# Kernel tuning notes

Hardware: AMD Instinct MI355X
Metric: run time of the kernel (lower is better)

The kernel has to match this reference:

```python
import jax, jax.numpy as jnp
import numpy as np
from jax import lax

DIM = 1024
BATCH = 16
WIDTH = 2048
DECAY = 0.99


def setup_inputs() -> dict:
    key = jax.random.key(0)
    k1, k2, k3, k4 = jax.random.split(key, 4)
    scale = 1.0 / np.sqrt(DIM)
    x = jax.random.normal(k1, (BATCH, WIDTH, DIM), dtype=jnp.float32)
    state = jnp.zeros((BATCH, DIM), dtype=jnp.float32)
    Wv = jax.random.normal(k2, (DIM, DIM), dtype=jnp.float32) * scale
    Wr = jax.random.normal(k3, (DIM, DIM), dtype=jnp.float32) * scale
    Wc = jax.random.normal(k4, (DIM, DIM), dtype=jnp.float32) * scale
    return {"x": x, "state": state, "Wv": Wv, "Wr": Wr, "Wc": Wc}


def reference(x, state, Wv, Wr, Wc):
    # x: [B, W, D], state: [B, D]; fixed-decay RWKV recurrence along width.
    decay = jnp.asarray(DECAY, dtype=x.dtype)
    one_minus = jnp.asarray(1.0, dtype=x.dtype) - decay
    v = jnp.einsum('bwd,de->bwe', x, Wv)                 # value projection
    r = jax.nn.sigmoid(jnp.einsum('bwd,de->bwe', x, Wr))  # receptance

    # scan over width (time) axis: elems shaped [W, B, D]
    def step(s_prev, inp):
        v_t, r_t, x_t = inp
        s_curr = decay * s_prev + one_minus * v_t
        y_t = x_t + r_t * s_curr
        return s_curr, y_t

    elems = (jnp.swapaxes(v, 0, 1), jnp.swapaxes(r, 0, 1), jnp.swapaxes(x, 0, 1))
    new_state, y_t = lax.scan(step, state, elems)
    y = jnp.swapaxes(y_t, 0, 1)                          # [B, W, D]
    y = y + jnp.einsum('bwd,de->bwe', y, Wc)             # minimal channel mix
    return y, new_state
```

## Files before the change

kernel.cpp:

```cpp
#include <hip/hip_runtime.h>
#include <hip/hip_bf16.h>
#include <math.h>


#define MROWS 32768
#define NCHUNK 16
#define CHUNKL 128
#define DECAY_F 0.99f
#define OM_F 0.01f

typedef __attribute__((ext_vector_type(8))) short short8;
typedef __attribute__((ext_vector_type(4))) float floatx4;

using bf16 = __hip_bfloat16;
using bf162 = __hip_bfloat162;

__device__ __forceinline__ void async_copy16(const bf16* g, bf16* l) {
  __builtin_amdgcn_global_load_lds(
      (const __attribute__((address_space(1))) unsigned int*)g,
      (__attribute__((address_space(3))) unsigned int*)l, 16, 0, 0);
}

__global__ void prep_x(const float* __restrict__ X, bf16* __restrict__ Xb) {
  const int idx = blockIdx.x * 256 + threadIdx.x;
  const float4 v = ((const float4*)X)[idx];
  union { ushort4 u; bf16 h[4]; } pk;
  pk.h[0] = __float2bfloat16(v.x);
  pk.h[1] = __float2bfloat16(v.y);
  pk.h[2] = __float2bfloat16(v.z);
  pk.h[3] = __float2bfloat16(v.w);
  ((ushort4*)Xb)[idx] = pk.u;
}

__global__ void prep_weights(const float* __restrict__ Wv,
                             const float* __restrict__ Wr,
                             const float* __restrict__ Wc,
                             bf16* __restrict__ WT) {
  __shared__ float tile[32][33];
  const int bk = blockIdx.x * 32;
  const int bn = blockIdx.y * 32;
  const float* src;
  int nbase = bn;
  if (bn < 1024)      { src = Wv; }
  else if (bn < 2048) { src = Wr; nbase = bn - 1024; }
  else                { src = Wc; nbase = bn - 2048; }
  const int tx = threadIdx.x;
  const int ty = threadIdx.y;
  #pragma unroll
  for (int i = ty; i < 32; i += 8)
    tile[i][tx] = src[(size_t)(bk + i) * 1024 + nbase + tx];
  __syncthreads();
  #pragma unroll
  for (int i = ty; i < 32; i += 8)
    WT[(size_t)(bn + i) * 1024 + bk + tx] = __float2bfloat16(tile[tx][i]);
}

__global__ __launch_bounds__(256, 3) void gemm_vr(const bf16* __restrict__ Xb,
                                                  const bf16* __restrict__ WT,
                                                  bf16* __restrict__ Vout,
                                                  bf16* __restrict__ Rout) {
  __shared__ bf16 As[128][32];
  __shared__ bf16 Bs[128][32];
  const int t = threadIdx.x;
  const int id = blockIdx.x;
  const int grp = id >> 3, xcd = id & 7;
  const int mt = ((grp >> 4) << 3) | xcd;
  const int nt = grp & 15;
  const int m0 = mt * 128;
  const int lane = t & 63, wave = t >> 6;
  const int wm = wave >> 1, wn = wave & 1;
  const int ln15 = lane & 15, qd = lane >> 4;

  const bf16* Asrc = Xb + (size_t)m0 * 1024;
  const bf16* Bsrc = WT + (size_t)(nt * 128) * 1024;

  const int srow = lane >> 2;
  const int skb  = (lane & 3) * 8;

  floatx4 acc[4][4];
  #pragma unroll
  for (int i = 0; i < 4; ++i)
    #pragma unroll
    for (int j = 0; j < 4; ++j) acc[i][j] = (floatx4){0.f, 0.f, 0.f, 0.f};

  for (int k0 = 0; k0 < 1024; k0 += 32) {
    #pragma unroll
    for (int s = 0; s < 2; ++s) {
      const int seg = wave * 2 + s;
      const size_t roff = (size_t)(seg * 16 + srow) * 1024 + k0 + skb;
      async_copy16(&Asrc[roff], &As[seg * 16][0]);
      async_copy16(&Bsrc[roff], &Bs[seg * 16][0]);
    }
    __syncthreads();
    short8 fa[4], fb[4];
    #pragma unroll
    for (int tm = 0; tm < 4; ++tm)
      fa[tm] = *(const short8*)&As[wm * 64 + tm * 16 + ln15][qd * 8];
    #pragma unroll
    for (int tn = 0; tn < 4; ++tn)
      fb[tn] = *(const short8*)&Bs[wn * 64 + tn * 16 + ln15][qd * 8];
    #pragma unroll
    for (int tm = 0; tm < 4; ++tm)
      #pragma unroll
      for (int tn = 0; tn < 4; ++tn)
        acc[tm][tn] = __builtin_amdgcn_mfma_f32_16x16x32_bf16(
            fa[tm], fb[tn], acc[tm][tn], 0, 0, 0);
    __syncthreads();
  }

  const bool isr = (nt >= 8);
  bf16* outp = isr ? Rout : Vout;
  const int nc0 = (nt & 7) * 128;
  #pragma unroll
  for (int tm = 0; tm < 4; ++tm) {
    #pragma unroll
    for (int i = 0; i < 4; ++i) {
      const int m_g = m0 + wm * 64 + tm * 16 + qd * 4 + i;
      const size_t rowoff = (size_t)m_g * 1024 + nc0;
      #pragma unroll
      for (int tn = 0; tn < 4; ++tn) {
        float cv = acc[tm][tn][i];
        if (isr) cv = 1.0f / (1.0f + __expf(-cv));
        outp[rowoff + wn * 64 + tn * 16 + ln15] = __float2bfloat16(cv);
      }
    }
  }
}

__global__ void scan_partial(const bf16* __restrict__ V, float* __restrict__ sl) {
  const int idx = blockIdx.x * 256 + threadIdx.x;
  const int d2 = idx & 511;
  const int c = (idx >> 9) & 15;
  const int b = idx >> 13;
  const bf162* V2 = (const bf162*)V;
  const size_t base = (size_t)(b * 2048 + c * 128) * 512 + d2;
  float s0 = 0.f, s1 = 0.f;
  for (int w = 0; w < CHUNKL; ++w) {
    const bf162 v = V2[base + (size_t)w * 512];
    s0 = DECAY_F * s0 + OM_F * __bfloat162float(v.x);
    s1 = DECAY_F * s1 + OM_F * __bfloat162float(v.y);
  }
  const int o = (b * 16 + c) * 1024 + d2 * 2;
  sl[o] = s0;
  sl[o + 1] = s1;
}

__global__ void scan_chunk(const float* __restrict__ state,
                           const float* __restrict__ sl,
                           float* __restrict__ sin_,
                           float* __restrict__ state_out,
                           float decayL) {
  const int idx = blockIdx.x * 256 + threadIdx.x;
  const int d = idx & 1023;
  const int b = idx >> 10;
  float s = state[idx];
  #pragma unroll
  for (int c = 0; c < NCHUNK; ++c) {
    const int o = (b * 16 + c) * 1024 + d;
    sin_[o] = s;
    s = decayL * s + sl[o];
  }
  state_out[idx] = s;
}

__global__ void scan_apply(const bf16* __restrict__ Xb,
                           const bf16* __restrict__ R,
                           const float* __restrict__ sin_,
                           bf16* __restrict__ VY) {
  const int idx = blockIdx.x * 256 + threadIdx.x;
  const int d2 = idx & 511;
  const int c = (idx >> 9) & 15;
  const int b = idx >> 13;
  const bf162* R2 = (const bf162*)R;
  const bf162* X2 = (const bf162*)Xb;
  bf162* VY2 = (bf162*)VY;
  const size_t base = (size_t)(b * 2048 + c * 128) * 512 + d2;
  const int so = (b * 16 + c) * 1024 + d2 * 2;
  float s0 = sin_[so], s1 = sin_[so + 1];
  for (int w = 0; w < CHUNKL; ++w) {
    const size_t off = base + (size_t)w * 512;
    const bf162 v = VY2[off];
    const bf162 r = R2[off];
    const bf162 xx = X2[off];
    s0 = DECAY_F * s0 + OM_F * __bfloat162float(v.x);
    s1 = DECAY_F * s1 + OM_F * __bfloat162float(v.y);
    const float y0 = __bfloat162float(xx.x) + __bfloat162float(r.x) * s0;
    const float y1 = __bfloat162float(xx.y) + __bfloat162float(r.y) * s1;
    bf162 o;
    o.x = __float2bfloat16(y0);
    o.y = __float2bfloat16(y1);
    VY2[off] = o;
  }
}

__global__ __launch_bounds__(256, 3) void gemm_mix(const bf16* __restrict__ Yt,
                                                   const bf16* __restrict__ WcT,
                                                   float* __restrict__ Out) {
  __shared__ bf16 As[128][32];
  __shared__ bf16 Bs[128][32];
  const int t = threadIdx.x;
  const int id = blockIdx.x;
  const int grp = id >> 3, xcd = id & 7;
  const int mt = ((grp >> 3) << 3) | xcd;
  const int nt = grp & 7;
  const int m0 = mt * 128;
  const int nc0 = nt * 128;
  const int lane = t & 63, wave = t >> 6;
  const int wm = wave >> 1, wn = wave & 1;
  const int ln15 = lane & 15, qd = lane >> 4;

  const bf16* Asrc = Yt + (size_t)m0 * 1024;
  const bf16* Bsrc = WcT + (size_t)nc0 * 1024;

  const int srow = lane >> 2;
  const int skb  = (lane & 3) * 8;

  floatx4 acc[4][4];
  #pragma unroll
  for (int i = 0; i < 4; ++i)
    #pragma unroll
    for (int j = 0; j < 4; ++j) acc[i][j] = (floatx4){0.f, 0.f, 0.f, 0.f};

  for (int k0 = 0; k0 < 1024; k0 += 32) {
    #pragma unroll
    for (int s = 0; s < 2; ++s) {
      const int seg = wave * 2 + s;
      const size_t roff = (size_t)(seg * 16 + srow) * 1024 + k0 + skb;
      async_copy16(&Asrc[roff], &As[seg * 16][0]);
      async_copy16(&Bsrc[roff], &Bs[seg * 16][0]);
    }
    __syncthreads();
    short8 fa[4], fb[4];
    #pragma unroll
    for (int tm = 0; tm < 4; ++tm)
      fa[tm] = *(const short8*)&As[wm * 64 + tm * 16 + ln15][qd * 8];
    #pragma unroll
    for (int tn = 0; tn < 4; ++tn)
      fb[tn] = *(const short8*)&Bs[wn * 64 + tn * 16 + ln15][qd * 8];
    #pragma unroll
    for (int tm = 0; tm < 4; ++tm)
      #pragma unroll
      for (int tn = 0; tn < 4; ++tn)
        acc[tm][tn] = __builtin_amdgcn_mfma_f32_16x16x32_bf16(
            fa[tm], fb[tn], acc[tm][tn], 0, 0, 0);
    __syncthreads();
  }

  #pragma unroll
  for (int tm = 0; tm < 4; ++tm) {
    #pragma unroll
    for (int i = 0; i < 4; ++i) {
      const int m_g = m0 + wm * 64 + tm * 16 + qd * 4 + i;
      const size_t rowoff = (size_t)m_g * 1024 + nc0;
      #pragma unroll
      for (int tn = 0; tn < 4; ++tn) {
        const size_t o = rowoff + wn * 64 + tn * 16 + ln15;
        Out[o] = __bfloat162float(Yt[o]) + acc[tm][tn][i];
      }
    }
  }
}

extern "C" void kernel_launch(void* const* d_in, const int* in_sizes, int n_in,
                              void* d_out, int out_size, void* d_ws, size_t ws_size,
                              hipStream_t stream) {
  const float* x     = (const float*)d_in[0];
  const float* state = (const float*)d_in[1];
  const float* Wv    = (const float*)d_in[2];
  const float* Wr    = (const float*)d_in[3];
  const float* Wc    = (const float*)d_in[4];

  float* y_out = (float*)d_out;
  float* state_out = y_out + (size_t)MROWS * 1024;

  char* ws = (char*)d_ws;
  bf16* WT   = (bf16*)ws;
  bf16* Xb   = (bf16*)(ws + ((size_t)6 << 20));
  bf16* Vbuf = (bf16*)(ws + ((size_t)70 << 20));
  bf16* Rbuf = (bf16*)(ws + ((size_t)134 << 20));
  float* sl  = (float*)(ws + ((size_t)198 << 20));
  float* sin_ = (float*)(ws + ((size_t)199 << 20));
  bf16* WcT = WT + (size_t)2048 * 1024;

  const float decayL = (float)pow(0.99, (double)CHUNKL);

  prep_x<<<32768, 256, 0, stream>>>(x, Xb);
  prep_weights<<<dim3(32, 96), dim3(32, 8), 0, stream>>>(Wv, Wr, Wc, WT);
  gemm_vr<<<4096, 256, 0, stream>>>(Xb, WT, Vbuf, Rbuf);
  scan_partial<<<512, 256, 0, stream>>>(Vbuf, sl);
  scan_chunk<<<64, 256, 0, stream>>>(state, sl, sin_, state_out, decayL);
  scan_apply<<<512, 256, 0, stream>>>(Xb, Rbuf, sin_, Vbuf);
  gemm_mix<<<2048, 256, 0, stream>>>(Vbuf, WcT, y_out);
}
```

Baseline: 529.4 us.

## Quantize value/receptance GEMM inputs to FP8 with scaled MFMA and widen scan vectors

Converts x and Wv/Wr to FP8 (weights pre-scaled by 16, undone via the MFMA scale operand) and switches gemm_vr to the 16x16x128 f8f6f4 scaled MFMA with a K-step of 128 and an XOR-swizzled LDS layout. This halves GEMM input bytes and raises matrix throughput per instruction. The scan kernels now process four channels per thread and scan_apply reads the fp32 x directly instead of the bf16 copy. The trade-off is a larger numeric error from FP8 inputs, which may approach the tolerance.

```diff
diff --git a/kernel.cpp b/kernel.cpp
--- a/kernel.cpp
+++ b/kernel.cpp
@@ -11,31 +11,40 @@
 
 typedef __attribute__((ext_vector_type(8))) short short8;
 typedef __attribute__((ext_vector_type(4))) float floatx4;
+typedef __attribute__((ext_vector_type(8))) int i32x8;
 
 using bf16 = __hip_bfloat16;
-using bf162 = __hip_bfloat162;
-
-__device__ __forceinline__ void async_copy16(const bf16* g, bf16* l) {
+
+__device__ __forceinline__ void async_copy16(const void* g, void* l) {
   __builtin_amdgcn_global_load_lds(
       (const __attribute__((address_space(1))) unsigned int*)g,
       (__attribute__((address_space(3))) unsigned int*)l, 16, 0, 0);
 }
 
-__global__ void prep_x(const float* __restrict__ X, bf16* __restrict__ Xb) {
+__device__ __forceinline__ float b2f(unsigned short u) {
+  union { unsigned int i; float f; } t; t.i = ((unsigned int)u) << 16; return t.f;
+}
+__device__ __forceinline__ unsigned short f2bu(float f) {
+  bf16 h = __float2bfloat16(f);
+  return *reinterpret_cast<unsigned short*>(&h);
+}
+
+__global__ void prep_x8(const float* __restrict__ X, unsigned char* __restrict__ Xq) {
   const int idx = blockIdx.x * 256 + threadIdx.x;
-  const float4 v = ((const float4*)X)[idx];
-  union { ushort4 u; bf16 h[4]; } pk;
-  pk.h[0] = __float2bfloat16(v.x);
-  pk.h[1] = __float2bfloat16(v.y);
-  pk.h[2] = __float2bfloat16(v.z);
-  pk.h[3] = __float2bfloat16(v.w);
-  ((ushort4*)Xb)[idx] = pk.u;
+  const float4 v0 = ((const float4*)X)[idx * 2];
+  const float4 v1 = ((const float4*)X)[idx * 2 + 1];
+  int p0 = __builtin_amdgcn_cvt_pk_fp8_f32(v0.x, v0.y, 0, false);
+  p0 = __builtin_amdgcn_cvt_pk_fp8_f32(v0.z, v0.w, p0, true);
+  int p1 = __builtin_amdgcn_cvt_pk_fp8_f32(v1.x, v1.y, 0, false);
+  p1 = __builtin_amdgcn_cvt_pk_fp8_f32(v1.z, v1.w, p1, true);
+  ((uint2*)Xq)[idx] = make_uint2((unsigned)p0, (unsigned)p1);
 }
 
 __global__ void prep_weights(const float* __restrict__ Wv,
                              const float* __restrict__ Wr,
                              const float* __restrict__ Wc,
-                             bf16* __restrict__ WT) {
+                             unsigned char* __restrict__ Wq8,
+                             bf16* __restrict__ WcT) {
   __shared__ float tile[32][33];
   const int bk = blockIdx.x * 32;
   const int bn = blockIdx.y * 32;
@@ -50,17 +59,25 @@
   for (int i = ty; i < 32; i += 8)
     tile[i][tx] = src[(size_t)(bk + i) * 1024 + nbase + tx];
   __syncthreads();
-  #pragma unroll
-  for (int i = ty; i < 32; i += 8)
-    WT[(size_t)(bn + i) * 1024 + bk + tx] = __float2bfloat16(tile[tx][i]);
-}
-
-__global__ __launch_bounds__(256, 3) void gemm_vr(const bf16* __restrict__ Xb,
-                                                  const bf16* __restrict__ WT,
+  if (bn < 2048) {
+    #pragma unroll
+    for (int i = ty; i < 32; i += 8) {
+      const int p = __builtin_amdgcn_cvt_pk_fp8_f32(tile[tx][i] * 16.0f, 0.f, 0, false);
+      Wq8[(size_t)(bn + i) * 1024 + bk + tx] = (unsigned char)(p & 0xff);
+    }
+  } else {
+    #pragma unroll
+    for (int i = ty; i < 32; i += 8)
+      WcT[(size_t)(bn - 2048 + i) * 1024 + bk + tx] = __float2bfloat16(tile[tx][i]);
+  }
+}
+
+__global__ __launch_bounds__(256, 3) void gemm_vr(const unsigned char* __restrict__ Xq,
+                                                  const unsigned char* __restrict__ Wq8,
                                                   bf16* __restrict__ Vout,
                                                   bf16* __restrict__ Rout) {
-  __shared__ bf16 As[128][32];
-  __shared__ bf16 Bs[128][32];
+  __shared__ uint4 As4[1024];
+  __shared__ uint4 Bs4[1024];
   const int t = threadIdx.x;
   const int id = blockIdx.x;
   const int grp = id >> 3, xcd = id & 7;
@@ -68,14 +85,15 @@
   const int nt = grp & 15;
   const int m0 = mt * 128;
   const int lane = t & 63, wave = t >> 6;
-  const int wm = wave >> 1, wn = wave & 1;
+  const int wm = (wave >> 1) * 64, wn = (wave & 1) * 64;
   const int ln15 = lane & 15, qd = lane >> 4;
-
-  const bf16* Asrc = Xb + (size_t)m0 * 1024;
-  const bf16* Bsrc = WT + (size_t)(nt * 128) * 1024;
-
-  const int srow = lane >> 2;
-  const int skb  = (lane & 3) * 8;
+  const int swz = ln15 & 7;
+
+  const unsigned char* Asrc = Xq + (size_t)m0 * 1024;
+  const unsigned char* Bsrc = Wq8 + (size_t)(nt * 128) * 1024;
+
+  const int r8 = lane >> 3;
+  const int xcol = ((lane & 7) ^ r8) * 16;
 
   floatx4 acc[4][4];
   #pragma unroll
@@ -83,28 +101,38 @@
     #pragma unroll
     for (int j = 0; j < 4; ++j) acc[i][j] = (floatx4){0.f, 0.f, 0.f, 0.f};
 
-  for (int k0 = 0; k0 < 1024; k0 += 32) {
-    #pragma unroll
-    for (int s = 0; s < 2; ++s) {
-      const int seg = wave * 2 + s;
-      const size_t roff = (size_t)(seg * 16 + srow) * 1024 + k0 + skb;
-      async_copy16(&Asrc[roff], &As[seg * 16][0]);
-      async_copy16(&Bsrc[roff], &Bs[seg * 16][0]);
+  for (int k0 = 0; k0 < 1024; k0 += 128) {
+    #pragma unroll
+    for (int c = 0; c < 4; ++c) {
+      const int rbase = wave * 32 + c * 8;
+      const size_t goff = (size_t)(rbase + r8) * 1024 + k0 + xcol;
+      async_copy16(Asrc + goff, (char*)&As4[rbase * 8]);
+      async_copy16(Bsrc + goff, (char*)&Bs4[rbase * 8]);
     }
     __syncthreads();
-    short8 fa[4], fb[4];
-    #pragma unroll
-    for (int tm = 0; tm < 4; ++tm)
-      fa[tm] = *(const short8*)&As[wm * 64 + tm * 16 + ln15][qd * 8];
-    #pragma unroll
-    for (int tn = 0; tn < 4; ++tn)
-      fb[tn] = *(const short8*)&Bs[wn * 64 + tn * 16 + ln15][qd * 8];
+    i32x8 fa[4], fb[4];
+    #pragma unroll
+    for (int tm = 0; tm < 4; ++tm) {
+      const int row = wm + tm * 16 + ln15;
+      const uint4 lo = As4[row * 8 + ((qd * 2) ^ swz)];
+      const uint4 hi = As4[row * 8 + ((qd * 2 + 1) ^ swz)];
+      fa[tm][0] = lo.x; fa[tm][1] = lo.y; fa[tm][2] = lo.z; fa[tm][3] = lo.w;
+      fa[tm][4] = hi.x; fa[tm][5] = hi.y; fa[tm][6] = hi.z; fa[tm][7] = hi.w;
+    }
+    #pragma unroll
+    for (int tn = 0; tn < 4; ++tn) {
+      const int row = wn + tn * 16 + ln15;
+      const uint4 lo = Bs4[row * 8 + ((qd * 2) ^ swz)];
+      const uint4 hi = Bs4[row * 8 + ((qd * 2 + 1) ^ swz)];
+      fb[tn][0] = lo.x; fb[tn][1] = lo.y; fb[tn][2] = lo.z; fb[tn][3] = lo.w;
+      fb[tn][4] = hi.x; fb[tn][5] = hi.y; fb[tn][6] = hi.z; fb[tn][7] = hi.w;
+    }
     #pragma unroll
     for (int tm = 0; tm < 4; ++tm)
       #pragma unroll
       for (int tn = 0; tn < 4; ++tn)
-        acc[tm][tn] = __builtin_amdgcn_mfma_f32_16x16x32_bf16(
-            fa[tm], fb[tn], acc[tm][tn], 0, 0, 0);
+        acc[tm][tn] = __builtin_amdgcn_mfma_scale_f32_16x16x128_f8f6f4(
+            fa[tm], fb[tn], acc[tm][tn], 0, 0, 0, 127, 0, 123);
     __syncthreads();
   }
 
@@ -115,13 +143,13 @@
   for (int tm = 0; tm < 4; ++tm) {
     #pragma unroll
     for (int i = 0; i < 4; ++i) {
-      const int m_g = m0 + wm * 64 + tm * 16 + qd * 4 + i;
+      const int m_g = m0 + wm + tm * 16 + qd * 4 + i;
       const size_t rowoff = (size_t)m_g * 1024 + nc0;
       #pragma unroll
       for (int tn = 0; tn < 4; ++tn) {
         float cv = acc[tm][tn][i];
         if (isr) cv = 1.0f / (1.0f + __expf(-cv));
-        outp[rowoff + wn * 64 + tn * 16 + ln15] = __float2bfloat16(cv);
+        outp[rowoff + wn + tn * 16 + ln15] = __float2bfloat16(cv);
       }
     }
   }
@@ -129,20 +157,20 @@
 
 __global__ void scan_partial(const bf16* __restrict__ V, float* __restrict__ sl) {
   const int idx = blockIdx.x * 256 + threadIdx.x;
-  const int d2 = idx & 511;
-  const int c = (idx >> 9) & 15;
-  const int b = idx >> 13;
-  const bf162* V2 = (const bf162*)V;
-  const size_t base = (size_t)(b * 2048 + c * 128) * 512 + d2;
-  float s0 = 0.f, s1 = 0.f;
+  const int d4 = idx & 255;
+  const int c = (idx >> 8) & 15;
+  const int b = idx >> 12;
+  const ushort4* V4 = (const ushort4*)V;
+  const size_t base = (size_t)(b * 2048 + c * 128) * 256 + d4;
+  float s0 = 0.f, s1 = 0.f, s2 = 0.f, s3 = 0.f;
   for (int w = 0; w < CHUNKL; ++w) {
-    const bf162 v = V2[base + (size_t)w * 512];
-    s0 = DECAY_F * s0 + OM_F * __bfloat162float(v.x);
-    s1 = DECAY_F * s1 + OM_F * __bfloat162float(v.y);
-  }
-  const int o = (b * 16 + c) * 1024 + d2 * 2;
-  sl[o] = s0;
-  sl[o + 1] = s1;
+    const ushort4 v = V4[base + (size_t)w * 256];
+    s0 = DECAY_F * s0 + OM_F * b2f(v.x);
+    s1 = DECAY_F * s1 + OM_F * b2f(v.y);
+    s2 = DECAY_F * s2 + OM_F * b2f(v.z);
+    s3 = DECAY_F * s3 + OM_F * b2f(v.w);
+  }
+  ((float4*)sl)[(b * 16 + c) * 256 + d4] = make_float4(s0, s1, s2, s3);
 }
 
 __global__ void scan_chunk(const float* __restrict__ state,
@@ -163,33 +191,34 @@
   state_out[idx] = s;
 }
 
-__global__ void scan_apply(const bf16* __restrict__ Xb,
+__global__ void scan_apply(const float* __restrict__ X,
                            const bf16* __restrict__ R,
                            const float* __restrict__ sin_,
                            bf16* __restrict__ VY) {
   const int idx = blockIdx.x * 256 + threadIdx.x;
-  const int d2 = idx & 511;
-  const int c = (idx >> 9) & 15;
-  const int b = idx >> 13;
-  const bf162* R2 = (const bf162*)R;
-  const bf162* X2 = (const bf162*)Xb;
-  bf162* VY2 = (bf162*)VY;
-  const size_t base = (size_t)(b * 2048 + c * 128) * 512 + d2;
-  const int so = (b * 16 + c) * 1024 + d2 * 2;
-  float s0 = sin_[so], s1 = sin_[so + 1];
+  const int d4 = idx & 255;
+  const int c = (idx >> 8) & 15;
+  const int b = idx >> 12;
+  const ushort4* R4 = (const ushort4*)R;
+  const float4* X4 = (const float4*)X;
+  ushort4* VY4 = (ushort4*)VY;
+  const size_t base = (size_t)(b * 2048 + c * 128) * 256 + d4;
+  float4 s = ((const float4*)sin_)[(b * 16 + c) * 256 + d4];
   for (int w = 0; w < CHUNKL; ++w) {
-    const size_t off = base + (size_t)w * 512;
-    const bf162 v = VY2[off];
-    const bf162 r = R2[off];
-    const bf162 xx = X2[off];
-    s0 = DECAY_F * s0 + OM_F * __bfloat162float(v.x);
-    s1 = DECAY_F * s1 + OM_F * __bfloat162float(v.y);
-    const float y0 = __bfloat162float(xx.x) + __bfloat162float(r.x) * s0;
-    const float y1 = __bfloat162float(xx.y) + __bfloat162float(r.y) * s1;
-    bf162 o;
-    o.x = __float2bfloat16(y0);
-    o.y = __float2bfloat16(y1);
-    VY2[off] = o;
+    const size_t off = base + (size_t)w * 256;
+    const ushort4 v = VY4[off];
+    const ushort4 r = R4[off];
+    const float4 xx = X4[off];
+    s.x = DECAY_F * s.x + OM_F * b2f(v.x);
+    s.y = DECAY_F * s.y + OM_F * b2f(v.y);
+    s.z = DECAY_F * s.z + OM_F * b2f(v.z);
+    s.w = DECAY_F * s.w + OM_F * b2f(v.w);
+    ushort4 o;
+    o.x = f2bu(xx.x + b2f(r.x) * s.x);
+    o.y = f2bu(xx.y + b2f(r.y) * s.y);
+    o.z = f2bu(xx.z + b2f(r.z) * s.z);
+    o.w = f2bu(xx.w + b2f(r.w) * s.w);
+    VY4[off] = o;
   }
 }
 
@@ -255,7 +284,7 @@
       #pragma unroll
       for (int tn = 0; tn < 4; ++tn) {
         const size_t o = rowoff + wn * 64 + tn * 16 + ln15;
-        Out[o] = __bfloat162float(Yt[o]) + acc[tm][tn][i];
+        Out[o] = b2f(*(const unsigned short*)&Yt[o]) + acc[tm][tn][i];
       }
     }
   }
@@ -274,21 +303,21 @@
   float* state_out = y_out + (size_t)MROWS * 1024;
 
   char* ws = (char*)d_ws;
-  bf16* WT   = (bf16*)ws;
-  bf16* Xb   = (bf16*)(ws + ((size_t)6 << 20));
-  bf16* Vbuf = (bf16*)(ws + ((size_t)70 << 20));
-  bf16* Rbuf = (bf16*)(ws + ((size_t)134 << 20));
-  float* sl  = (float*)(ws + ((size_t)198 << 20));
-  float* sin_ = (float*)(ws + ((size_t)199 << 20));
-  bf16* WcT = WT + (size_t)2048 * 1024;
+  unsigned char* Wq8 = (unsigned char*)ws;
+  bf16* WcT  = (bf16*)(ws + ((size_t)2 << 20));
+  unsigned char* Xq  = (unsigned char*)(ws + ((size_t)4 << 20));
+  bf16* Vbuf = (bf16*)(ws + ((size_t)36 << 20));
+  bf16* Rbuf = (bf16*)(ws + ((size_t)100 << 20));
+  float* sl  = (float*)(ws + ((size_t)164 << 20));
+  float* sin_ = (float*)(ws + ((size_t)165 << 20));
 
   const float decayL = (float)pow(0.99, (double)CHUNKL);
 
-  prep_x<<<32768, 256, 0, stream>>>(x, Xb);
-  prep_weights<<<dim3(32, 96), dim3(32, 8), 0, stream>>>(Wv, Wr, Wc, WT);
-  gemm_vr<<<4096, 256, 0, stream>>>(Xb, WT, Vbuf, Rbuf);
-  scan_partial<<<512, 256, 0, stream>>>(Vbuf, sl);
+  prep_x8<<<16384, 256, 0, stream>>>(x, Xq);
+  prep_weights<<<dim3(32, 96), dim3(32, 8), 0, stream>>>(Wv, Wr, Wc, Wq8, WcT);
+  gemm_vr<<<4096, 256, 0, stream>>>(Xq, Wq8, Vbuf, Rbuf);
+  scan_partial<<<256, 256, 0, stream>>>(Vbuf, sl);
   scan_chunk<<<64, 256, 0, stream>>>(state, sl, sin_, state_out, decayL);
-  scan_apply<<<512, 256, 0, stream>>>(Xb, Rbuf, sin_, Vbuf);
+  scan_apply<<<256, 256, 0, stream>>>(x, Rbuf, sin_, Vbuf);
   gemm_mix<<<2048, 256, 0, stream>>>(Vbuf, WcT, y_out);
 }
```

Result: slower. 1.340 ms (+153.1%).
